# Performance work log

Measured on AMD Instinct MI355X. Metric: run time of the kernel, lower is better.

## Reference

```python
import jax, jax.numpy as jnp
import numpy as np

B, S, H = 8, 4096, 2048
TOP_K = 32


def setup_inputs() -> dict:
    key = jax.random.key(0)
    k1, k2, k3 = jax.random.split(key, 3)
    base = jax.random.normal(k1, (B, S, H), dtype=jnp.float32)
    batch_weights = jax.random.normal(k2, (B, 1, H), dtype=jnp.float32)
    intervention_positions = jax.random.randint(k3, (B, S), 0, S, dtype=jnp.int32)
    return {"base": base, "intervention_positions": intervention_positions,
            "batch_weights": batch_weights}


def reference(base, intervention_positions, batch_weights):
    # base: [B,S,H]; intervention_positions: [B,S]; batch_weights: [B,1,H]
    b, s, h = base.shape
    bidx = jnp.arange(b)[:, None]                                   # [B,1]
    # gather intervened hidden states: base[b, pos]  -> [B,S,H]
    gathered = jnp.take_along_axis(base, intervention_positions[..., None], axis=1)
    # psi(h) = ReLU(W h): rank-1 bmm with batch_weights -> [B,S]
    detect_latent = jax.nn.relu(
        jnp.einsum('bsh,bh->bs', gathered, batch_weights[:, 0, :]))
    topk_vals, topk_idx = jax.lax.top_k(detect_latent, TOP_K)       # [B,K]
    # zero out the top-k entries (scatter along last dim)
    non_topk_latents = detect_latent.at[bidx, topk_idx].set(0.0)
    # steering vector: mean(topk) * W  -> [B,1,H]
    steer = jnp.mean(topk_vals, axis=-1)[:, None, None] * batch_weights
    # scatter-add steering vector back at the intervened positions
    mixed_output = base.at[bidx, intervention_positions].add(
        jnp.broadcast_to(steer, (b, s, h)))
    return mixed_output, detect_latent, non_topk_latents
```

## Files before the change

### kernel.cpp

```cpp
#include <hip/hip_runtime.h>

#define TOPK 32

typedef float vfloat4 __attribute__((ext_vector_type(4)));

__global__ void hist_kernel(const int* __restrict__ pos,
                            int* __restrict__ counts,
                            int S) {
    extern __shared__ int cnt[];
    int b = blockIdx.x;
    int t = threadIdx.x;
    for (int i = t; i < S; i += 256) cnt[i] = 0;
    __syncthreads();
    for (int i = t; i < S; i += 256)
        atomicAdd(&cnt[pos[(size_t)b * S + i]], 1);
    __syncthreads();
    for (int i = t; i < S; i += 256)
        counts[(size_t)b * S + i] = cnt[i];
}

__global__ void dot_kernel(const float* __restrict__ base,
                           const float* __restrict__ bw,
                           const int* __restrict__ counts,
                           float* __restrict__ d2,
                           int S, int H) {
    int wid  = (blockIdx.x * blockDim.x + threadIdx.x) >> 6;
    int lane = threadIdx.x & 63;
    if (counts[wid] == 0) return;
    int b = wid / S;

    const float4* row = (const float4*)(base + (size_t)wid * H);
    const float4* w4  = (const float4*)(bw + (size_t)b * H);
    int n4 = H >> 2;

    float acc = 0.f;
    #pragma unroll 8
    for (int i = lane; i < n4; i += 64) {
        float4 v = row[i];
        float4 w = w4[i];
        acc += v.x * w.x + v.y * w.y + v.z * w.z + v.w * w.w;
    }
    #pragma unroll
    for (int off = 32; off > 0; off >>= 1)
        acc += __shfl_down(acc, off, 64);

    if (lane == 0) d2[wid] = acc;
}

__global__ void topk_copy_kernel(const float* __restrict__ d2,
                                 const int* __restrict__ pos,
                                 const int* __restrict__ counts,
                                 const float* __restrict__ base,
                                 float* __restrict__ mixed,
                                 float* __restrict__ detect,
                                 float* __restrict__ nontopk,
                                 float* __restrict__ meanv,
                                 int B, int S, int H, int nblocks) {
    __shared__ float smem[8192];
    int t = threadIdx.x;

    if (blockIdx.x < B) {
        float* dvals = smem;
        float* vals  = smem + S;
        int b = blockIdx.x;

        for (int i = t; i < S; i += 256)
            dvals[i] = d2[(size_t)b * S + i];
        __syncthreads();
        for (int i = t; i < S; i += 256) {
            float v = fmaxf(dvals[pos[(size_t)b * S + i]], 0.f);
            vals[i] = v;
            detect[(size_t)b * S + i] = v;
        }
        __syncthreads();

        if (t < 64) {
            int lane = t;
            float sum = 0.f;
            for (int it = 0; it < TOPK; ++it) {
                float lv = -INFINITY;
                int   li = 0x7fffffff;
                for (int c = lane * 4; c < S; c += 256) {
                    float4 v = *(const float4*)&vals[c];
                    if (v.x > lv) { lv = v.x; li = c; }
                    if (v.y > lv) { lv = v.y; li = c + 1; }
                    if (v.z > lv) { lv = v.z; li = c + 2; }
                    if (v.w > lv) { lv = v.w; li = c + 3; }
                }
                #pragma unroll
                for (int off = 32; off > 0; off >>= 1) {
                    float ov = __shfl_down(lv, off, 64);
                    int   oi = __shfl_down(li, off, 64);
                    if (ov > lv || (ov == lv && oi < li)) { lv = ov; li = oi; }
                }
                lv = __shfl(lv, 0, 64);
                li = __shfl(li, 0, 64);
                sum += lv;
                if (lane == 0) vals[li] = -INFINITY;
            }
            if (lane == 0) meanv[b] = sum / (float)TOPK;
        }
        __syncthreads();
        for (int i = t; i < S; i += 256) {
            float v = vals[i];
            nontopk[(size_t)b * S + i] = (v == -INFINITY) ? 0.f : v;
        }
    } else {
        int nrows = B * S;
        int ncopy = nblocks - B;
        int n4 = H >> 2;
        for (int row = blockIdx.x - B; row < nrows; row += ncopy) {
            if (counts[row] != 0) continue;
            const vfloat4* bp = (const vfloat4*)(base + (size_t)row * H);
            vfloat4*       op = (vfloat4*)(mixed + (size_t)row * H);
            #pragma unroll 2
            for (int i = t; i < n4; i += 256) {
                vfloat4 v = __builtin_nontemporal_load(&bp[i]);
                __builtin_nontemporal_store(v, &op[i]);
            }
        }
    }
}

__global__ void mix_kernel(const float* __restrict__ base,
                           const float* __restrict__ bw,
                           const int* __restrict__ counts,
                           const float* __restrict__ meanv,
                           float* __restrict__ mixed,
                           int S, int H) {
    int r0 = blockIdx.x << 2;
    int b  = r0 / S;
    const float4* w4 = (const float4*)(bw + (size_t)b * H);
    float mb = meanv[b];
    int n4 = H >> 2;

    for (int r = r0; r < r0 + 4; ++r) {
        int c = counts[r];
        if (c == 0) continue;
        float scale = (float)c * mb;
        const float4* b4 = (const float4*)(base + (size_t)r * H);
        vfloat4*      o4 = (vfloat4*)(mixed + (size_t)r * H);
        #pragma unroll 2
        for (int i = threadIdx.x; i < n4; i += blockDim.x) {
            float4 v = b4[i];
            float4 w = w4[i];
            vfloat4 o;
            o.x = v.x + scale * w.x;
            o.y = v.y + scale * w.y;
            o.z = v.z + scale * w.z;
            o.w = v.w + scale * w.w;
            __builtin_nontemporal_store(o, &o4[i]);
        }
    }
}

extern "C" void kernel_launch(void* const* d_in, const int* in_sizes, int n_in,
                              void* d_out, int out_size, void* d_ws, size_t ws_size,
                              hipStream_t stream) {
    const float* base = (const float*)d_in[0];
    const int*   pos  = (const int*)d_in[1];
    const float* bw   = (const float*)d_in[2];

    long n0 = in_sizes[0];
    long n1 = in_sizes[1];
    long n2 = in_sizes[2];
    int H = (int)(n0 / n1);
    int B = (int)(n2 / H);
    int S = (int)(n1 / B);

    float* out_mixed   = (float*)d_out;
    float* out_detect  = out_mixed + (size_t)B * S * H;
    float* out_nontopk = out_detect + (size_t)B * S;

    int*   counts = (int*)d_ws;
    float* d2     = (float*)((char*)d_ws + (size_t)B * S * sizeof(int));
    float* meanv  = (float*)((char*)d_ws + 2 * (size_t)B * S * sizeof(int));

    int nrows = B * S;
    int nk2   = B + 1024;

    hist_kernel<<<B, 256, (size_t)S * sizeof(int), stream>>>(pos, counts, S);
    dot_kernel<<<nrows / 4, 256, 0, stream>>>(base, bw, counts, d2, S, H);
    topk_copy_kernel<<<nk2, 256, 0, stream>>>(
        d2, pos, counts, base, out_mixed, out_detect, out_nontopk, meanv,
        B, S, H, nk2);
    mix_kernel<<<nrows / 4, 256, 0, stream>>>(base, bw, counts, meanv, out_mixed, S, H);
}
```

Measured before the change: 166.3 us.

## Fuse mix kernel into topk/copy kernel with a global done-flag barrier

Merges the separate mix kernel into the top-k/copy kernel. Copy blocks first copy untouched rows, then spin on a global atomic counter until all B top-k blocks have published meanv, and then apply the steering add to intervened rows. The aim is to remove one kernel launch and the idle gap between the copy and mix phases. In exchange it adds a memset, a spin-wait inter-block dependency that relies on all 1024 blocks being co-resident to avoid deadlock, and a launch-bounds hint.

```diff
diff --git a/kernel.cpp b/kernel.cpp
--- a/kernel.cpp
+++ b/kernel.cpp
@@ -47,17 +47,22 @@
     if (lane == 0) d2[wid] = acc;
 }
 
-__global__ void topk_copy_kernel(const float* __restrict__ d2,
-                                 const int* __restrict__ pos,
-                                 const int* __restrict__ counts,
-                                 const float* __restrict__ base,
-                                 float* __restrict__ mixed,
-                                 float* __restrict__ detect,
-                                 float* __restrict__ nontopk,
-                                 float* __restrict__ meanv,
-                                 int B, int S, int H, int nblocks) {
+__global__ __launch_bounds__(256, 4)
+void topk_copy_mix_kernel(const float* __restrict__ d2,
+                          const int* __restrict__ pos,
+                          const int* __restrict__ counts,
+                          const float* __restrict__ base,
+                          const float* __restrict__ bw,
+                          float* __restrict__ mixed,
+                          float* __restrict__ detect,
+                          float* __restrict__ nontopk,
+                          float* __restrict__ meanv,
+                          int* __restrict__ done,
+                          int B, int S, int H, int ncopy) {
     __shared__ float smem[8192];
-    int t = threadIdx.x;
+    const int t = threadIdx.x;
+    const int n4 = H >> 2;
+    const int nrows = B * S;
 
     if (blockIdx.x < B) {
         float* dvals = smem;
@@ -101,15 +106,19 @@
             if (lane == 0) meanv[b] = sum / (float)TOPK;
         }
         __syncthreads();
+        if (t == 0) {
+            __threadfence();
+            __hip_atomic_fetch_add(done, 1, __ATOMIC_RELEASE,
+                                   __HIP_MEMORY_SCOPE_AGENT);
+        }
         for (int i = t; i < S; i += 256) {
             float v = vals[i];
             nontopk[(size_t)b * S + i] = (v == -INFINITY) ? 0.f : v;
         }
     } else {
-        int nrows = B * S;
-        int ncopy = nblocks - B;
-        int n4 = H >> 2;
-        for (int row = blockIdx.x - B; row < nrows; row += ncopy) {
+        const int start = blockIdx.x - B;
+
+        for (int row = start; row < nrows; row += ncopy) {
             if (counts[row] != 0) continue;
             const vfloat4* bp = (const vfloat4*)(base + (size_t)row * H);
             vfloat4*       op = (vfloat4*)(mixed + (size_t)row * H);
@@ -119,37 +128,33 @@
                 __builtin_nontemporal_store(v, &op[i]);
             }
         }
-    }
-}
 
-__global__ void mix_kernel(const float* __restrict__ base,
-                           const float* __restrict__ bw,
-                           const int* __restrict__ counts,
-                           const float* __restrict__ meanv,
-                           float* __restrict__ mixed,
-                           int S, int H) {
-    int r0 = blockIdx.x << 2;
-    int b  = r0 / S;
-    const float4* w4 = (const float4*)(bw + (size_t)b * H);
-    float mb = meanv[b];
-    int n4 = H >> 2;
+        if (t == 0) {
+            while (__hip_atomic_load(done, __ATOMIC_ACQUIRE,
+                                     __HIP_MEMORY_SCOPE_AGENT) < B)
+                __builtin_amdgcn_s_sleep(16);
+        }
+        __syncthreads();
 
-    for (int r = r0; r < r0 + 4; ++r) {
-        int c = counts[r];
-        if (c == 0) continue;
-        float scale = (float)c * mb;
-        const float4* b4 = (const float4*)(base + (size_t)r * H);
-        vfloat4*      o4 = (vfloat4*)(mixed + (size_t)r * H);
-        #pragma unroll 2
-        for (int i = threadIdx.x; i < n4; i += blockDim.x) {
-            float4 v = b4[i];
-            float4 w = w4[i];
-            vfloat4 o;
-            o.x = v.x + scale * w.x;
-            o.y = v.y + scale * w.y;
-            o.z = v.z + scale * w.z;
-            o.w = v.w + scale * w.w;
-            __builtin_nontemporal_store(o, &o4[i]);
+        for (int row = start; row < nrows; row += ncopy) {
+            int c = counts[row];
+            if (c == 0) continue;
+            int b = row / S;
+            float scale = (float)c * meanv[b];
+            const float4* bp = (const float4*)(base + (size_t)row * H);
+            const float4* wp = (const float4*)(bw + (size_t)b * H);
+            vfloat4*      op = (vfloat4*)(mixed + (size_t)row * H);
+            #pragma unroll 2
+            for (int i = t; i < n4; i += 256) {
+                float4 v = bp[i];
+                float4 w = wp[i];
+                vfloat4 o;
+                o.x = v.x + scale * w.x;
+                o.y = v.y + scale * w.y;
+                o.z = v.z + scale * w.z;
+                o.w = v.w + scale * w.w;
+                __builtin_nontemporal_store(o, &op[i]);
+            }
         }
     }
 }
@@ -172,17 +177,19 @@
     float* out_detect  = out_mixed + (size_t)B * S * H;
     float* out_nontopk = out_detect + (size_t)B * S;
 
-    int*   counts = (int*)d_ws;
-    float* d2     = (float*)((char*)d_ws + (size_t)B * S * sizeof(int));
-    float* meanv  = (float*)((char*)d_ws + 2 * (size_t)B * S * sizeof(int));
+    int*   done   = (int*)d_ws;
+    int*   counts = done + 16;
+    float* d2     = (float*)(counts + (size_t)B * S);
+    float* meanv  = d2 + (size_t)B * S;
 
     int nrows = B * S;
-    int nk2   = B + 1024;
+    int ncopy = 1016;
+    int grid2 = B + ncopy;
 
+    hipMemsetAsync(done, 0, 16 * sizeof(int), stream);
     hist_kernel<<<B, 256, (size_t)S * sizeof(int), stream>>>(pos, counts, S);
     dot_kernel<<<nrows / 4, 256, 0, stream>>>(base, bw, counts, d2, S, H);
-    topk_copy_kernel<<<nk2, 256, 0, stream>>>(
-        d2, pos, counts, base, out_mixed, out_detect, out_nontopk, meanv,
-        B, S, H, nk2);
-    mix_kernel<<<nrows / 4, 256, 0, stream>>>(base, bw, counts, meanv, out_mixed, S, H);
+    topk_copy_mix_kernel<<<grid2, 256, 0, stream>>>(
+        d2, pos, counts, base, bw, out_mixed, out_detect, out_nontopk,
+        meanv, done, B, S, H, ncopy);
 }
```

Result: slower. 201.1 us (+20.9%).

## Compact referenced and unreferenced row lists to avoid idle waves in dot/mix/copy

Applied to the files above, without the earlier changes.

The histogram kernel now also builds per-batch compacted lists of referenced rows and unreferenced rows with a block prefix scan. The dot and mix kernels index through the referenced list, and the copy blocks walk the unreferenced list, so no waves are launched and then idled on rows they skip. This is meant to remove divergence and wasted wave scheduling, since roughly 37% of rows are never referenced. In exchange it adds an indirection load per row, a 2D grid with many early-exit blocks, and a serial per-thread chunk scan inside the histogram kernel.

```diff
diff --git a/kernel.cpp b/kernel.cpp
--- a/kernel.cpp
+++ b/kernel.cpp
@@ -4,58 +4,88 @@
 
 typedef float vfloat4 __attribute__((ext_vector_type(4)));
 
-__global__ void hist_kernel(const int* __restrict__ pos,
-                            int* __restrict__ counts,
-                            int S) {
+__global__ void hist_compact_kernel(const int* __restrict__ pos,
+                                    int* __restrict__ counts,
+                                    int* __restrict__ refList,
+                                    int* __restrict__ zeroList,
+                                    int* __restrict__ nrefb,
+                                    int S) {
     extern __shared__ int cnt[];
-    int b = blockIdx.x;
-    int t = threadIdx.x;
+    __shared__ int partial[256];
+    int b = blockIdx.x, t = threadIdx.x;
+    const int CH = S >> 8;
+
     for (int i = t; i < S; i += 256) cnt[i] = 0;
     __syncthreads();
     for (int i = t; i < S; i += 256)
         atomicAdd(&cnt[pos[(size_t)b * S + i]], 1);
     __syncthreads();
-    for (int i = t; i < S; i += 256)
-        counts[(size_t)b * S + i] = cnt[i];
+
+    int base_i = t * CH;
+    int loc = 0;
+    for (int k = 0; k < CH; ++k) loc += (cnt[base_i + k] > 0);
+    partial[t] = loc;
+    __syncthreads();
+    for (int off = 1; off < 256; off <<= 1) {
+        int add = (t >= off) ? partial[t - off] : 0;
+        __syncthreads();
+        partial[t] += add;
+        __syncthreads();
+    }
+    int excl = partial[t] - loc;
+
+    int run = 0;
+    for (int k = 0; k < CH; ++k) {
+        int i = base_i + k;
+        int c = cnt[i];
+        counts[(size_t)b * S + i] = c;
+        int refpos = excl + run;
+        if (c > 0) { refList[(size_t)b * S + refpos] = i; ++run; }
+        else       { zeroList[(size_t)b * S + (i - refpos)] = i; }
+    }
+    if (t == 255) nrefb[b] = partial[255];
 }
 
 __global__ void dot_kernel(const float* __restrict__ base,
                            const float* __restrict__ bw,
-                           const int* __restrict__ counts,
+                           const int* __restrict__ refList,
+                           const int* __restrict__ nrefb,
                            float* __restrict__ d2,
                            int S, int H) {
-    int wid  = (blockIdx.x * blockDim.x + threadIdx.x) >> 6;
+    int b = blockIdx.y;
+    int j = blockIdx.x * 4 + (threadIdx.x >> 6);
+    if (j >= nrefb[b]) return;
     int lane = threadIdx.x & 63;
-    if (counts[wid] == 0) return;
-    int b = wid / S;
-
-    const float4* row = (const float4*)(base + (size_t)wid * H);
-    const float4* w4  = (const float4*)(bw + (size_t)b * H);
+    int row = b * S + refList[(size_t)b * S + j];
+
+    const float4* rp = (const float4*)(base + (size_t)row * H);
+    const float4* wp = (const float4*)(bw + (size_t)b * H);
     int n4 = H >> 2;
 
     float acc = 0.f;
     #pragma unroll 8
     for (int i = lane; i < n4; i += 64) {
-        float4 v = row[i];
-        float4 w = w4[i];
+        float4 v = rp[i];
+        float4 w = wp[i];
         acc += v.x * w.x + v.y * w.y + v.z * w.z + v.w * w.w;
     }
     #pragma unroll
     for (int off = 32; off > 0; off >>= 1)
         acc += __shfl_down(acc, off, 64);
 
-    if (lane == 0) d2[wid] = acc;
+    if (lane == 0) d2[row] = acc;
 }
 
 __global__ void topk_copy_kernel(const float* __restrict__ d2,
                                  const int* __restrict__ pos,
-                                 const int* __restrict__ counts,
+                                 const int* __restrict__ zeroList,
+                                 const int* __restrict__ nrefb,
                                  const float* __restrict__ base,
                                  float* __restrict__ mixed,
                                  float* __restrict__ detect,
                                  float* __restrict__ nontopk,
                                  float* __restrict__ meanv,
-                                 int B, int S, int H, int nblocks) {
+                                 int B, int S, int H, int ncopy) {
     __shared__ float smem[8192];
     int t = threadIdx.x;
 
@@ -106,17 +136,19 @@
             nontopk[(size_t)b * S + i] = (v == -INFINITY) ? 0.f : v;
         }
     } else {
-        int nrows = B * S;
-        int ncopy = nblocks - B;
         int n4 = H >> 2;
-        for (int row = blockIdx.x - B; row < nrows; row += ncopy) {
-            if (counts[row] != 0) continue;
-            const vfloat4* bp = (const vfloat4*)(base + (size_t)row * H);
-            vfloat4*       op = (vfloat4*)(mixed + (size_t)row * H);
-            #pragma unroll 2
-            for (int i = t; i < n4; i += 256) {
-                vfloat4 v = __builtin_nontemporal_load(&bp[i]);
-                __builtin_nontemporal_store(v, &op[i]);
+        int start = blockIdx.x - B;
+        for (int b = 0; b < B; ++b) {
+            int nz = S - nrefb[b];
+            for (int j = start; j < nz; j += ncopy) {
+                int row = b * S + zeroList[(size_t)b * S + j];
+                const vfloat4* bp = (const vfloat4*)(base + (size_t)row * H);
+                vfloat4*       op = (vfloat4*)(mixed + (size_t)row * H);
+                #pragma unroll 2
+                for (int i = t; i < n4; i += 256) {
+                    vfloat4 v = __builtin_nontemporal_load(&bp[i]);
+                    __builtin_nontemporal_store(v, &op[i]);
+                }
             }
         }
     }
@@ -124,32 +156,38 @@
 
 __global__ void mix_kernel(const float* __restrict__ base,
                            const float* __restrict__ bw,
+                           const int* __restrict__ refList,
+                           const int* __restrict__ nrefb,
                            const int* __restrict__ counts,
                            const float* __restrict__ meanv,
                            float* __restrict__ mixed,
                            int S, int H) {
-    int r0 = blockIdx.x << 2;
-    int b  = r0 / S;
-    const float4* w4 = (const float4*)(bw + (size_t)b * H);
+    int b = blockIdx.y;
+    int nr = nrefb[b];
+    int j0 = blockIdx.x << 2;
+    if (j0 >= nr) return;
     float mb = meanv[b];
+    const float4* wp = (const float4*)(bw + (size_t)b * H);
     int n4 = H >> 2;
 
-    for (int r = r0; r < r0 + 4; ++r) {
-        int c = counts[r];
-        if (c == 0) continue;
-        float scale = (float)c * mb;
-        const float4* b4 = (const float4*)(base + (size_t)r * H);
-        vfloat4*      o4 = (vfloat4*)(mixed + (size_t)r * H);
+    #pragma unroll
+    for (int k = 0; k < 4; ++k) {
+        int j = j0 + k;
+        if (j >= nr) break;
+        int row = b * S + refList[(size_t)b * S + j];
+        float scale = (float)counts[row] * mb;
+        const float4* bp = (const float4*)(base + (size_t)row * H);
+        vfloat4*      op = (vfloat4*)(mixed + (size_t)row * H);
         #pragma unroll 2
         for (int i = threadIdx.x; i < n4; i += blockDim.x) {
-            float4 v = b4[i];
-            float4 w = w4[i];
+            float4 v = bp[i];
+            float4 w = wp[i];
             vfloat4 o;
             o.x = v.x + scale * w.x;
             o.y = v.y + scale * w.y;
             o.z = v.z + scale * w.z;
             o.w = v.w + scale * w.w;
-            __builtin_nontemporal_store(o, &o4[i]);
+            __builtin_nontemporal_store(o, &op[i]);
         }
     }
 }
@@ -172,17 +210,23 @@
     float* out_detect  = out_mixed + (size_t)B * S * H;
     float* out_nontopk = out_detect + (size_t)B * S;
 
-    int*   counts = (int*)d_ws;
-    float* d2     = (float*)((char*)d_ws + (size_t)B * S * sizeof(int));
-    float* meanv  = (float*)((char*)d_ws + 2 * (size_t)B * S * sizeof(int));
-
-    int nrows = B * S;
-    int nk2   = B + 1024;
-
-    hist_kernel<<<B, 256, (size_t)S * sizeof(int), stream>>>(pos, counts, S);
-    dot_kernel<<<nrows / 4, 256, 0, stream>>>(base, bw, counts, d2, S, H);
-    topk_copy_kernel<<<nk2, 256, 0, stream>>>(
-        d2, pos, counts, base, out_mixed, out_detect, out_nontopk, meanv,
-        B, S, H, nk2);
-    mix_kernel<<<nrows / 4, 256, 0, stream>>>(base, bw, counts, meanv, out_mixed, S, H);
-}
+    size_t BS = (size_t)B * S;
+    int*   nrefb    = (int*)d_ws;
+    int*   counts   = nrefb + 16;
+    int*   refList  = counts + BS;
+    int*   zeroList = refList + BS;
+    float* d2       = (float*)(zeroList + BS);
+    float* meanv    = d2 + BS;
+
+    int ncopy = 1016;
+    dim3 grid2d(S / 4, B);
+
+    hist_compact_kernel<<<B, 256, (size_t)S * sizeof(int), stream>>>(
+        pos, counts, refList, zeroList, nrefb, S);
+    dot_kernel<<<grid2d, 256, 0, stream>>>(base, bw, refList, nrefb, d2, S, H);
+    topk_copy_kernel<<<B + ncopy, 256, 0, stream>>>(
+        d2, pos, zeroList, nrefb, base, out_mixed, out_detect, out_nontopk,
+        meanv, B, S, H, ncopy);
+    mix_kernel<<<grid2d, 256, 0, stream>>>(
+        base, bw, refList, nrefb, counts, meanv, out_mixed, S, H);
+}
```

Measured after the change: 173.5 us. 4.3% more time.
